# Performance work log

Measured on AMD Instinct MI355X. Metric: run time of the kernel, lower is better.

The kernel has to match this reference:

```python
import jax, jax.numpy as jnp
import numpy as np

H = 1024  # hidden_size


def setup_inputs() -> dict:
    key = jax.random.key(0)
    ks = jax.random.split(key, 8)
    B, T = 256, 512
    s = 1.0 / np.sqrt(H)  # torch nn.RNN / nn.Linear default init scale
    return {
        "initial_input": jax.random.normal(ks[0], (B, 1), jnp.float32),
        "hidden": jax.random.normal(ks[1], (B, H), jnp.float32),
        "targets": jax.random.normal(ks[2], (T, B, 1), jnp.float32),
        "W_ih": jax.random.uniform(ks[3], (H, 1), jnp.float32, -s, s),
        "W_hh": jax.random.uniform(ks[4], (H, H), jnp.float32, -s, s),
        "b_ih": jax.random.uniform(ks[5], (H,), jnp.float32, -s, s),
        "b_hh": jax.random.uniform(ks[6], (H,), jnp.float32, -s, s),
        "W_out": jax.random.uniform(ks[7], (1, H), jnp.float32, -s, s),
        "b_out": jnp.zeros((1,), jnp.float32),
        "teacher_force_probability": 1,
    }


def reference(initial_input, hidden, targets, W_ih, W_hh, b_ih, b_hh, W_out, b_out,
              teacher_force_probability):
    # teacher_force_probability == 1 -> always teacher-forced: input at step t is
    # targets[t-1], with initial_input at t=0 (deterministic version of random()<p).
    xs = jnp.concatenate([initial_input[None], targets[:-1]], axis=0)  # [T, B, 1]

    def step(h, x):
        # Elman RNN cell: h' = tanh(x W_ih^T + b_ih + h W_hh^T + b_hh)
        h = jnp.tanh(x @ W_ih.T + b_ih + h @ W_hh.T + b_hh)  # [B, H]
        y = h @ W_out.T + b_out                               # [B, 1]
        return h, y

    _, outputs = jax.lax.scan(step, hidden, xs)  # outputs: [T, B, 1]
    return outputs
```

## Files before the change

### kernel.cpp

```cpp
#include <hip/hip_runtime.h>

#define TT 512
#define BATCH 256
#define HH 1024

typedef _Float16 half4  __attribute__((ext_vector_type(4)));
typedef _Float16 half8  __attribute__((ext_vector_type(8)));
typedef float    floatx4 __attribute__((ext_vector_type(4)));
typedef unsigned uint4v  __attribute__((ext_vector_type(4)));
typedef unsigned long long u64;
typedef u64 u64x2 __attribute__((ext_vector_type(2)));

__device__ __forceinline__ u64 hload(const _Float16* p) {
    return __hip_atomic_load((const u64*)p, __ATOMIC_RELAXED, __HIP_MEMORY_SCOPE_AGENT);
}
__device__ __forceinline__ void hstore(_Float16* p, u64 v) {
    __hip_atomic_store((u64*)p, v, __ATOMIC_RELAXED, __HIP_MEMORY_SCOPE_AGENT);
}

template<bool FAST>
__device__ __forceinline__ void run_steps(
    int bbq, int jb, int tid, int w, int l15, int lhi,
    const float* __restrict__ x0, const float* __restrict__ targets,
    float* __restrict__ out,
    _Float16* __restrict__ hbuf0, _Float16* __restrict__ hbuf1,
    unsigned* __restrict__ cnt, unsigned* __restrict__ flags,
    const half8 (&wfrag)[2][32], int e0, int e1,
    float bias0, float bias1, float wih0, float wih1,
    float wout0, float wout1, float bout,
    float* x_lds, float* y_red, _Float16* hlds, char* hstage_b)
{
    for (int s = 0; s < TT; ++s) {
        const _Float16* hs = (s & 1) ? hbuf1 : hbuf0;
        _Float16*       hd = (s & 1) ? hbuf0 : hbuf1;

        float xval = 0.f;
        if (tid < 16)
            xval = (s == 0) ? x0[bbq * 16 + tid]
                            : targets[(size_t)(s - 1) * BATCH + bbq * 16 + tid];

        if (tid == 0) {
            if (FAST) {
                const unsigned tgt = (unsigned)s;
                for (;;) {
                    uint4v a = *(volatile const uint4v*)&flags[bbq * 8];
                    uint4v b = *(volatile const uint4v*)&flags[bbq * 8 + 4];
                    unsigned m = a[0];
                    m = m < a[1] ? m : a[1]; m = m < a[2] ? m : a[2];
                    m = m < a[3] ? m : a[3]; m = m < b[0] ? m : b[0];
                    m = m < b[1] ? m : b[1]; m = m < b[2] ? m : b[2];
                    m = m < b[3] ? m : b[3];
                    if (m >= tgt) break;
                }
            } else {
                const unsigned tgt = 8u * (unsigned)(s + 1);
                while (__hip_atomic_load(&cnt[bbq], __ATOMIC_RELAXED,
                                         __HIP_MEMORY_SCOPE_AGENT) < tgt) {}
            }
        }
        if (tid < 16) x_lds[tid] = xval;
        __syncthreads();
        __builtin_amdgcn_sched_barrier(0);

        if (FAST) {
            const char* gsrc = (const char*)(hs + (size_t)bbq * 16 * HH);
            u64x2 sv[8];
            #pragma unroll
            for (int i = 0; i < 8; ++i) {
                const int c = tid + i * 256;
                sv[i] = *(volatile const u64x2*)(gsrc + (c >> 7) * 2048 + (c & 127) * 16);
            }
            __builtin_amdgcn_sched_barrier(0);
            #pragma unroll
            for (int i = 0; i < 8; ++i) {
                const int c = tid + i * 256;
                const int row = c >> 7, colb = (c & 127) * 16;
                *(u64x2*)(hstage_b + row * 2048 + (colb ^ ((row & 7) << 4))) = sv[i];
            }
        } else {
            const _Float16* sb = hs + (size_t)bbq * 16 * HH;
            u64 sv[16];
            #pragma unroll
            for (int r = 0; r < 16; ++r)
                sv[r] = hload(sb + r * HH + tid * 4);
            __builtin_amdgcn_sched_barrier(0);
            #pragma unroll
            for (int r = 0; r < 16; ++r)
                *(u64*)(hstage_b + r * 2048 + ((tid * 8) ^ ((r & 7) << 4))) = sv[r];
        }
        __syncthreads();

        floatx4 a00 = {0,0,0,0}, a01 = {0,0,0,0}, a10 = {0,0,0,0}, a11 = {0,0,0,0};
        #pragma unroll
        for (int t = 0; t < 16; ++t) {
            const half8 av0 = *(const half8*)(hstage_b + e0 + t * 128);
            const half8 av1 = *(const half8*)(hstage_b + e1 + t * 128);
            a00 = __builtin_amdgcn_mfma_f32_16x16x32_f16(av0, wfrag[0][2 * t],     a00, 0, 0, 0);
            a10 = __builtin_amdgcn_mfma_f32_16x16x32_f16(av0, wfrag[1][2 * t],     a10, 0, 0, 0);
            a01 = __builtin_amdgcn_mfma_f32_16x16x32_f16(av1, wfrag[0][2 * t + 1], a01, 0, 0, 0);
            a11 = __builtin_amdgcn_mfma_f32_16x16x32_f16(av1, wfrag[1][2 * t + 1], a11, 0, 0, 0);
        }
        const floatx4 xv = *(const floatx4*)&x_lds[lhi * 4];

        float ht0[4], ht1[4];
        #pragma unroll
        for (int r = 0; r < 4; ++r) {
            const float p0 = a00[r] + a01[r] + bias0 + xv[r] * wih0;
            const float p1 = a10[r] + a11[r] + bias1 + xv[r] * wih1;
            const float ex0 = __expf(2.0f * p0);
            const float ex1 = __expf(2.0f * p1);
            ht0[r] = 1.0f - 2.0f / (ex0 + 1.0f);
            ht1[r] = 1.0f - 2.0f / (ex1 + 1.0f);
        }

        #pragma unroll
        for (int r = 0; r < 4; ++r) {
            hlds[(lhi * 4 + r) * 128 + (w * 16 + l15)]      = (_Float16)ht0[r];
            hlds[(lhi * 4 + r) * 128 + (w * 16 + l15) + 64] = (_Float16)ht1[r];
        }

        float yv[4];
        #pragma unroll
        for (int r = 0; r < 4; ++r) yv[r] = ht0[r] * wout0 + ht1[r] * wout1;
        #pragma unroll
        for (int off = 1; off < 16; off <<= 1) {
            #pragma unroll
            for (int r = 0; r < 4; ++r) yv[r] += __shfl_xor(yv[r], off);
        }
        if (l15 == 0) {
            #pragma unroll
            for (int r = 0; r < 4; ++r) y_red[w * 16 + lhi * 4 + r] = yv[r];
        }
        __syncthreads();

        if (tid < 64) {
            if (FAST) {
                #pragma unroll
                for (int c = 0; c < 4; ++c) {
                    const int q   = tid + c * 64;
                    const int row = q >> 4, ch = q & 15;
                    u64x2 v = *(const u64x2*)&hlds[row * 128 + ch * 8];
                    *(u64x2*)(hd + (size_t)(bbq * 16 + row) * HH + jb * 128 + ch * 8) = v;
                }
                asm volatile("s_waitcnt vmcnt(0)" ::: "memory");
                if (tid == 0)
                    *(volatile unsigned*)&flags[bbq * 8 + jb] = (unsigned)(s + 1);
            } else {
                #pragma unroll
                for (int c = 0; c < 8; ++c) {
                    const int q   = tid + c * 64;
                    const int row = q >> 5, cc = q & 31;
                    u64 v = *(const u64*)&hlds[row * 128 + cc * 4];
                    hstore(hd + (size_t)(bbq * 16 + row) * HH + jb * 128 + cc * 4, v);
                }
                asm volatile("s_waitcnt vmcnt(0)" ::: "memory");
                if (tid == 0)
                    __hip_atomic_fetch_add(&cnt[bbq], 1u, __ATOMIC_RELAXED,
                                           __HIP_MEMORY_SCOPE_AGENT);
            }
        }

        if (tid >= 64 && tid < 80) {
            const int b = tid - 64;
            const float y = y_red[0 * 16 + b] + y_red[1 * 16 + b] +
                            y_red[2 * 16 + b] + y_red[3 * 16 + b] + bout;
            atomicAdd(&out[(size_t)s * BATCH + bbq * 16 + b], y);
        }
    }
}

__global__ __launch_bounds__(256, 1)
void rnn_persistent(const float* __restrict__ x0,
                    const float* __restrict__ hidden0,
                    const float* __restrict__ targets,
                    const float* __restrict__ W_ih,
                    const float* __restrict__ W_hh,
                    const float* __restrict__ b_ih,
                    const float* __restrict__ b_hh,
                    const float* __restrict__ W_out,
                    const float* __restrict__ b_out,
                    float*       __restrict__ out,
                    _Float16*    __restrict__ hbuf0,
                    _Float16*    __restrict__ hbuf1,
                    unsigned*    __restrict__ cnt,
                    unsigned*    __restrict__ flags,
                    unsigned*    __restrict__ xcds)
{
    const int wg  = blockIdx.x;
    const int bbq = wg & 15;
    const int jb  = wg >> 4;
    const int tid = threadIdx.x;
    const int w   = tid >> 6;
    const int l   = tid & 63;
    const int l15 = l & 15;
    const int lhi = l >> 4;

    __shared__ __align__(16) float    x_lds[16];
    __shared__ __align__(16) float    y_red[4 * 16];
    __shared__ __align__(16) _Float16 hlds[16 * 128];
    __shared__ __align__(16) _Float16 hstage[16 * 1024];
    __shared__            int         fastflag;

    unsigned xcc;
    asm volatile("s_getreg_b32 %0, hwreg(HW_REG_XCC_ID)" : "=s"(xcc));

    const int   jcol0  = jb * 128 + w * 16 + l15;
    const int   jcol1  = jcol0 + 64;

    half8 wfrag[2][32];
    #pragma unroll
    for (int c = 0; c < 2; ++c) {
        const float* wr = W_hh + (size_t)(c ? jcol1 : jcol0) * HH + lhi * 8;
        #pragma unroll
        for (int kk = 0; kk < 32; ++kk) {
            floatx4 lo = *(const floatx4*)(wr + kk * 32);
            floatx4 hi = *(const floatx4*)(wr + kk * 32 + 4);
            half8 f;
            f[0]=(_Float16)lo[0]; f[1]=(_Float16)lo[1]; f[2]=(_Float16)lo[2]; f[3]=(_Float16)lo[3];
            f[4]=(_Float16)hi[0]; f[5]=(_Float16)hi[1]; f[6]=(_Float16)hi[2]; f[7]=(_Float16)hi[3];
            wfrag[c][kk] = f;
        }
    }

    const float bias0  = b_ih[jcol0] + b_hh[jcol0];
    const float bias1  = b_ih[jcol1] + b_hh[jcol1];
    const float wih0   = W_ih[jcol0], wih1 = W_ih[jcol1];
    const float wout0  = W_out[jcol0], wout1 = W_out[jcol1];
    const float bout   = (jb == 0) ? b_out[0] : 0.f;

    const int xm = (l15 & 7) << 4;
    const int e0 = l15 * 2048 + ((lhi * 16) ^ xm);
    const int e1 = l15 * 2048 + ((64 + lhi * 16) ^ xm);
    char* hstage_b = (char*)hstage;

    #pragma unroll
    for (int c = 0; c < 2; ++c) {
        const int q   = tid + c * 256;
        const int row = q >> 5, cc = q & 31;
        const float* s = hidden0 + (size_t)(bbq * 16 + row) * HH + jb * 128 + cc * 4;
        floatx4 f4 = *(const floatx4*)s;
        half4 h4;
        h4[0]=(_Float16)f4[0]; h4[1]=(_Float16)f4[1]; h4[2]=(_Float16)f4[2]; h4[3]=(_Float16)f4[3];
        hstore(hbuf0 + (size_t)(bbq * 16 + row) * HH + jb * 128 + cc * 4,
               __builtin_bit_cast(u64, h4));
    }
    if (tid == 0)
        __hip_atomic_store(&xcds[wg], xcc, __ATOMIC_RELAXED, __HIP_MEMORY_SCOPE_AGENT);
    asm volatile("s_waitcnt vmcnt(0)" ::: "memory");
    __syncthreads();
    if (tid == 0)
        __hip_atomic_fetch_add(&cnt[bbq], 1u, __ATOMIC_RELAXED, __HIP_MEMORY_SCOPE_AGENT);

    if (tid == 0) {
        while (__hip_atomic_load(&cnt[bbq], __ATOMIC_RELAXED,
                                 __HIP_MEMORY_SCOPE_AGENT) < 8u) {}
    }
    __syncthreads();
    if (tid < 64) {
        unsigned v = 0;
        if (l < 8)
            v = __hip_atomic_load(&xcds[(l << 4) + bbq], __ATOMIC_RELAXED,
                                  __HIP_MEMORY_SCOPE_AGENT);
        const unsigned v0 = __shfl(v, 0);
        const bool ok = (l >= 8) || (v == v0);
        const unsigned long long m = __ballot(ok);
        if (tid == 0) fastflag = (m == ~0ull) ? 1 : 0;
    }
    __syncthreads();
    const bool fast = (fastflag != 0);

    if (fast)
        run_steps<true >(bbq, jb, tid, w, l15, lhi, x0, targets, out,
                         hbuf0, hbuf1, cnt, flags, wfrag, e0, e1,
                         bias0, bias1, wih0, wih1, wout0, wout1, bout,
                         x_lds, y_red, hlds, hstage_b);
    else
        run_steps<false>(bbq, jb, tid, w, l15, lhi, x0, targets, out,
                         hbuf0, hbuf1, cnt, flags, wfrag, e0, e1,
                         bias0, bias1, wih0, wih1, wout0, wout1, bout,
                         x_lds, y_red, hlds, hstage_b);
}

extern "C" void kernel_launch(void* const* d_in, const int* in_sizes, int n_in,
                              void* d_out, int out_size, void* d_ws, size_t ws_size,
                              hipStream_t stream)
{
    const float* x0      = (const float*)d_in[0];
    const float* hidden0 = (const float*)d_in[1];
    const float* targets = (const float*)d_in[2];
    const float* W_ih    = (const float*)d_in[3];
    const float* W_hh    = (const float*)d_in[4];
    const float* b_ih    = (const float*)d_in[5];
    const float* b_hh    = (const float*)d_in[6];
    const float* W_out   = (const float*)d_in[7];
    const float* b_out   = (const float*)d_in[8];
    float* out = (float*)d_out;

    char* ws = (char*)d_ws;
    unsigned* cnt   = (unsigned*)ws;
    unsigned* flags = (unsigned*)(ws + 256);
    unsigned* xcds  = (unsigned*)(ws + 1024);
    _Float16* hbuf0 = (_Float16*)(ws + 4096);
    _Float16* hbuf1 = (_Float16*)(ws + 4096 + 512 * 1024);

    hipMemsetAsync(ws, 0, 4096, stream);
    hipMemsetAsync(d_out, 0, (size_t)out_size * sizeof(float), stream);

    rnn_persistent<<<128, 256, 0, stream>>>(x0, hidden0, targets, W_ih, W_hh,
                                            b_ih, b_hh, W_out, b_out,
                                            out, hbuf0, hbuf1, cnt, flags, xcds);
}
```

Before: 1.949 ms.

## Load hidden state directly into MFMA B-fragments and split K across wave pairs

Each wave now reads its slice of the previous hidden state straight from global memory into MFMA operand registers, with W_hh as the A operand. This removes the per-step LDS staging copy of the full 16x1024 h tile and one block barrier. The K dimension is split across pairs of waves, which combine partial sums through a small LDS exchange. Each wave then writes its tanh results directly to global memory instead of going through an LDS h tile, shortening the per-step critical path. The cost is more redundant global loads (each wave pair reloads the same h rows) and an added cross-wave reduction.

```diff
diff --git a/kernel.cpp b/kernel.cpp
--- a/kernel.cpp
+++ b/kernel.cpp
@@ -25,11 +25,17 @@
     float* __restrict__ out,
     _Float16* __restrict__ hbuf0, _Float16* __restrict__ hbuf1,
     unsigned* __restrict__ cnt, unsigned* __restrict__ flags,
-    const half8 (&wfrag)[2][32], int e0, int e1,
-    float bias0, float bias1, float wih0, float wih1,
-    float wout0, float wout1, float bout,
-    float* x_lds, float* y_red, _Float16* hlds, char* hstage_b)
+    const half8 (&wfrag)[4][16],
+    const float (&bias_r)[2][4], const float (&wih_r)[2][4],
+    const float (&wout_r)[2][4], float bout,
+    float* x_lds, floatx4* red, float* y_red)
 {
+    const int p   = w >> 1;
+    const int kh  = w & 1;
+    const int kb0 = kh ? 2 : 0;
+    const int sb0 = kh ? 0 : 2;
+    const int l   = tid & 63;
+
     for (int s = 0; s < TT; ++s) {
         const _Float16* hs = (s & 1) ? hbuf1 : hbuf0;
         _Float16*       hd = (s & 1) ? hbuf0 : hbuf1;
@@ -62,108 +68,87 @@
         __syncthreads();
         __builtin_amdgcn_sched_barrier(0);
 
-        if (FAST) {
-            const char* gsrc = (const char*)(hs + (size_t)bbq * 16 * HH);
-            u64x2 sv[8];
-            #pragma unroll
-            for (int i = 0; i < 8; ++i) {
-                const int c = tid + i * 256;
-                sv[i] = *(volatile const u64x2*)(gsrc + (c >> 7) * 2048 + (c & 127) * 16);
-            }
-            __builtin_amdgcn_sched_barrier(0);
-            #pragma unroll
-            for (int i = 0; i < 8; ++i) {
-                const int c = tid + i * 256;
-                const int row = c >> 7, colb = (c & 127) * 16;
-                *(u64x2*)(hstage_b + row * 2048 + (colb ^ ((row & 7) << 4))) = sv[i];
-            }
-        } else {
-            const _Float16* sb = hs + (size_t)bbq * 16 * HH;
-            u64 sv[16];
-            #pragma unroll
-            for (int r = 0; r < 16; ++r)
-                sv[r] = hload(sb + r * HH + tid * 4);
-            __builtin_amdgcn_sched_barrier(0);
-            #pragma unroll
-            for (int r = 0; r < 16; ++r)
-                *(u64*)(hstage_b + r * 2048 + ((tid * 8) ^ ((r & 7) << 4))) = sv[r];
-        }
-        __syncthreads();
-
-        floatx4 a00 = {0,0,0,0}, a01 = {0,0,0,0}, a10 = {0,0,0,0}, a11 = {0,0,0,0};
-        #pragma unroll
-        for (int t = 0; t < 16; ++t) {
-            const half8 av0 = *(const half8*)(hstage_b + e0 + t * 128);
-            const half8 av1 = *(const half8*)(hstage_b + e1 + t * 128);
-            a00 = __builtin_amdgcn_mfma_f32_16x16x32_f16(av0, wfrag[0][2 * t],     a00, 0, 0, 0);
-            a10 = __builtin_amdgcn_mfma_f32_16x16x32_f16(av0, wfrag[1][2 * t],     a10, 0, 0, 0);
-            a01 = __builtin_amdgcn_mfma_f32_16x16x32_f16(av1, wfrag[0][2 * t + 1], a01, 0, 0, 0);
-            a11 = __builtin_amdgcn_mfma_f32_16x16x32_f16(av1, wfrag[1][2 * t + 1], a11, 0, 0, 0);
-        }
-        const floatx4 xv = *(const floatx4*)&x_lds[lhi * 4];
-
-        float ht0[4], ht1[4];
-        #pragma unroll
-        for (int r = 0; r < 4; ++r) {
-            const float p0 = a00[r] + a01[r] + bias0 + xv[r] * wih0;
-            const float p1 = a10[r] + a11[r] + bias1 + xv[r] * wih1;
-            const float ex0 = __expf(2.0f * p0);
-            const float ex1 = __expf(2.0f * p1);
-            ht0[r] = 1.0f - 2.0f / (ex0 + 1.0f);
-            ht1[r] = 1.0f - 2.0f / (ex1 + 1.0f);
-        }
-
-        #pragma unroll
-        for (int r = 0; r < 4; ++r) {
-            hlds[(lhi * 4 + r) * 128 + (w * 16 + l15)]      = (_Float16)ht0[r];
-            hlds[(lhi * 4 + r) * 128 + (w * 16 + l15) + 64] = (_Float16)ht1[r];
-        }
-
-        float yv[4];
-        #pragma unroll
-        for (int r = 0; r < 4; ++r) yv[r] = ht0[r] * wout0 + ht1[r] * wout1;
-        #pragma unroll
-        for (int off = 1; off < 16; off <<= 1) {
-            #pragma unroll
-            for (int r = 0; r < 4; ++r) yv[r] += __shfl_xor(yv[r], off);
-        }
-        if (l15 == 0) {
-            #pragma unroll
-            for (int r = 0; r < 4; ++r) y_red[w * 16 + lhi * 4 + r] = yv[r];
-        }
-        __syncthreads();
-
-        if (tid < 64) {
+        const _Float16* hrow = hs + (size_t)(bbq * 16 + l15) * HH + kh * 512 + lhi * 8;
+        floatx4 acc[4] = {{0,0,0,0},{0,0,0,0},{0,0,0,0},{0,0,0,0}};
+        #pragma unroll
+        for (int half = 0; half < 2; ++half) {
+            half8 bfrag[8];
             if (FAST) {
                 #pragma unroll
-                for (int c = 0; c < 4; ++c) {
-                    const int q   = tid + c * 64;
-                    const int row = q >> 4, ch = q & 15;
-                    u64x2 v = *(const u64x2*)&hlds[row * 128 + ch * 8];
-                    *(u64x2*)(hd + (size_t)(bbq * 16 + row) * HH + jb * 128 + ch * 8) = v;
-                }
-                asm volatile("s_waitcnt vmcnt(0)" ::: "memory");
-                if (tid == 0)
-                    *(volatile unsigned*)&flags[bbq * 8 + jb] = (unsigned)(s + 1);
+                for (int t = 0; t < 8; ++t)
+                    bfrag[t] = __builtin_bit_cast(half8,
+                        *(volatile const u64x2*)(hrow + (half * 8 + t) * 32));
             } else {
                 #pragma unroll
-                for (int c = 0; c < 8; ++c) {
-                    const int q   = tid + c * 64;
-                    const int row = q >> 5, cc = q & 31;
-                    u64 v = *(const u64*)&hlds[row * 128 + cc * 4];
-                    hstore(hd + (size_t)(bbq * 16 + row) * HH + jb * 128 + cc * 4, v);
+                for (int t = 0; t < 8; ++t) {
+                    u64x2 v;
+                    v[0] = hload(hrow + (half * 8 + t) * 32);
+                    v[1] = hload(hrow + (half * 8 + t) * 32 + 4);
+                    bfrag[t] = __builtin_bit_cast(half8, v);
                 }
-                asm volatile("s_waitcnt vmcnt(0)" ::: "memory");
-                if (tid == 0)
-                    __hip_atomic_fetch_add(&cnt[bbq], 1u, __ATOMIC_RELAXED,
-                                           __HIP_MEMORY_SCOPE_AGENT);
-            }
-        }
-
+            }
+            #pragma unroll
+            for (int t = 0; t < 8; ++t) {
+                #pragma unroll
+                for (int b = 0; b < 4; ++b)
+                    acc[b] = __builtin_amdgcn_mfma_f32_16x16x32_f16(
+                        wfrag[b][half * 8 + t], bfrag[t], acc[b], 0, 0, 0);
+            }
+        }
+
+        red[(p * 4 + sb0)     * 64 + l] = acc[sb0];
+        red[(p * 4 + sb0 + 1) * 64 + l] = acc[sb0 + 1];
+        __syncthreads();
+        floatx4 pre0 = acc[kb0]     + red[(p * 4 + kb0)     * 64 + l];
+        floatx4 pre1 = acc[kb0 + 1] + red[(p * 4 + kb0 + 1) * 64 + l];
+
+        const float xb = x_lds[l15];
+        float ht[2][4];
+        #pragma unroll
+        for (int b2 = 0; b2 < 2; ++b2) {
+            const floatx4 pre = b2 ? pre1 : pre0;
+            #pragma unroll
+            for (int r = 0; r < 4; ++r) {
+                const float pp = pre[r] + bias_r[b2][r] + xb * wih_r[b2][r];
+                const float ex = __expf(2.0f * pp);
+                ht[b2][r] = 1.0f - 2.0f / (ex + 1.0f);
+            }
+        }
+
+        _Float16* hrd = hd + (size_t)(bbq * 16 + l15) * HH + jb * 128 + p * 64 + lhi * 4;
+        #pragma unroll
+        for (int b2 = 0; b2 < 2; ++b2) {
+            half4 hv;
+            hv[0] = (_Float16)ht[b2][0]; hv[1] = (_Float16)ht[b2][1];
+            hv[2] = (_Float16)ht[b2][2]; hv[3] = (_Float16)ht[b2][3];
+            if (FAST)
+                *(half4*)(hrd + (kb0 + b2) * 16) = hv;
+            else
+                hstore(hrd + (kb0 + b2) * 16, __builtin_bit_cast(u64, hv));
+        }
+
+        float yv = 0.f;
+        #pragma unroll
+        for (int b2 = 0; b2 < 2; ++b2)
+            #pragma unroll
+            for (int r = 0; r < 4; ++r)
+                yv += ht[b2][r] * wout_r[b2][r];
+        yv += __shfl_xor(yv, 16);
+        yv += __shfl_xor(yv, 32);
+        if (l < 16) y_red[w * 16 + l] = yv;
+
+        asm volatile("s_waitcnt vmcnt(0)" ::: "memory");
+        __syncthreads();
+        if (tid == 0) {
+            if (FAST)
+                *(volatile unsigned*)&flags[bbq * 8 + jb] = (unsigned)(s + 1);
+            else
+                __hip_atomic_fetch_add(&cnt[bbq], 1u, __ATOMIC_RELAXED,
+                                       __HIP_MEMORY_SCOPE_AGENT);
+        }
         if (tid >= 64 && tid < 80) {
             const int b = tid - 64;
-            const float y = y_red[0 * 16 + b] + y_red[1 * 16 + b] +
-                            y_red[2 * 16 + b] + y_red[3 * 16 + b] + bout;
+            const float y = y_red[b] + y_red[16 + b] + y_red[32 + b] + y_red[48 + b] + bout;
             atomicAdd(&out[(size_t)s * BATCH + bbq * 16 + b], y);
         }
     }
@@ -194,44 +179,45 @@
     const int l   = tid & 63;
     const int l15 = l & 15;
     const int lhi = l >> 4;
-
-    __shared__ __align__(16) float    x_lds[16];
-    __shared__ __align__(16) float    y_red[4 * 16];
-    __shared__ __align__(16) _Float16 hlds[16 * 128];
-    __shared__ __align__(16) _Float16 hstage[16 * 1024];
-    __shared__            int         fastflag;
+    const int p   = w >> 1;
+    const int kh  = w & 1;
+    const int kb0 = kh ? 2 : 0;
+
+    __shared__ __align__(16) float   x_lds[16];
+    __shared__ __align__(16) floatx4 red[2 * 4 * 64];
+    __shared__ __align__(16) float   y_red[4 * 16];
+    __shared__            int        fastflag;
 
     unsigned xcc;
     asm volatile("s_getreg_b32 %0, hwreg(HW_REG_XCC_ID)" : "=s"(xcc));
 
-    const int   jcol0  = jb * 128 + w * 16 + l15;
-    const int   jcol1  = jcol0 + 64;
-
-    half8 wfrag[2][32];
+    half8 wfrag[4][16];
     #pragma unroll
-    for (int c = 0; c < 2; ++c) {
-        const float* wr = W_hh + (size_t)(c ? jcol1 : jcol0) * HH + lhi * 8;
-        #pragma unroll
-        for (int kk = 0; kk < 32; ++kk) {
-            floatx4 lo = *(const floatx4*)(wr + kk * 32);
-            floatx4 hi = *(const floatx4*)(wr + kk * 32 + 4);
+    for (int b = 0; b < 4; ++b) {
+        const float* wr = W_hh + (size_t)(jb * 128 + p * 64 + b * 16 + l15) * HH
+                         + kh * 512 + lhi * 8;
+        #pragma unroll
+        for (int t = 0; t < 16; ++t) {
+            floatx4 lo = *(const floatx4*)(wr + t * 32);
+            floatx4 hi = *(const floatx4*)(wr + t * 32 + 4);
             half8 f;
             f[0]=(_Float16)lo[0]; f[1]=(_Float16)lo[1]; f[2]=(_Float16)lo[2]; f[3]=(_Float16)lo[3];
             f[4]=(_Float16)hi[0]; f[5]=(_Float16)hi[1]; f[6]=(_Float16)hi[2]; f[7]=(_Float16)hi[3];
-            wfrag[c][kk] = f;
-        }
-    }
-
-    const float bias0  = b_ih[jcol0] + b_hh[jcol0];
-    const float bias1  = b_ih[jcol1] + b_hh[jcol1];
-    const float wih0   = W_ih[jcol0], wih1 = W_ih[jcol1];
-    const float wout0  = W_out[jcol0], wout1 = W_out[jcol1];
-    const float bout   = (jb == 0) ? b_out[0] : 0.f;
-
-    const int xm = (l15 & 7) << 4;
-    const int e0 = l15 * 2048 + ((lhi * 16) ^ xm);
-    const int e1 = l15 * 2048 + ((64 + lhi * 16) ^ xm);
-    char* hstage_b = (char*)hstage;
+            wfrag[b][t] = f;
+        }
+    }
+
+    float bias_r[2][4], wih_r[2][4], wout_r[2][4];
+    #pragma unroll
+    for (int b2 = 0; b2 < 2; ++b2)
+        #pragma unroll
+        for (int r = 0; r < 4; ++r) {
+            const int j = jb * 128 + p * 64 + (kb0 + b2) * 16 + lhi * 4 + r;
+            bias_r[b2][r] = b_ih[j] + b_hh[j];
+            wih_r[b2][r]  = W_ih[j];
+            wout_r[b2][r] = W_out[j];
+        }
+    const float bout = (jb == 0) ? b_out[0] : 0.f;
 
     #pragma unroll
     for (int c = 0; c < 2; ++c) {
@@ -271,14 +257,12 @@
 
     if (fast)
         run_steps<true >(bbq, jb, tid, w, l15, lhi, x0, targets, out,
-                         hbuf0, hbuf1, cnt, flags, wfrag, e0, e1,
-                         bias0, bias1, wih0, wih1, wout0, wout1, bout,
-                         x_lds, y_red, hlds, hstage_b);
+                         hbuf0, hbuf1, cnt, flags, wfrag,
+                         bias_r, wih_r, wout_r, bout, x_lds, red, y_red);
     else
         run_steps<false>(bbq, jb, tid, w, l15, lhi, x0, targets, out,
-                         hbuf0, hbuf1, cnt, flags, wfrag, e0, e1,
-                         bias0, bias1, wih0, wih1, wout0, wout1, bout,
-                         x_lds, y_red, hlds, hstage_b);
+                         hbuf0, hbuf1, cnt, flags, wfrag,
+                         bias_r, wih_r, wout_r, bout, x_lds, red, y_red);
 }
 
 extern "C" void kernel_launch(void* const* d_in, const int* in_sizes, int n_in,
```

Result: slower. 2.826 ms (+45.0%).
